# Performance work log

Measured on AMD Instinct MI355X. Metric: run time of the kernel, lower is better.

## Reference

```python
import jax, jax.numpy as jnp
import numpy as np

MARGIN = 0.35
SCALE = 64.0
EPS = 1e-8  # torch F.cosine_similarity norm clamp


def setup_inputs() -> dict:
    key = jax.random.key(0)
    k1, k2 = jax.random.split(key)
    N, D = 8192, 512
    embeddings = jax.random.normal(k1, (N, D), dtype=jnp.float32)
    labels = jax.random.randint(k2, (N,), 0, 128, dtype=jnp.int64)
    return {"embeddings": embeddings, "labels": labels}


def reference(embeddings, labels):
    # cosine similarity as Gram matrix of norm-clamped-normalized rows
    norms = jnp.maximum(jnp.linalg.norm(embeddings, axis=1, keepdims=True), EPS)
    e = embeddings / norms                      # [N, D]
    sim = jnp.einsum('id,jd->ij', e, e)         # [N, N]
    pos_mask = (labels[:, None] == labels[None, :]).astype(sim.dtype)
    # pos_sim - neg_sim = sim*mask - sim*(1-mask) = sim*(2*mask - 1)
    signed = sim * (2.0 * pos_mask - 1.0)
    loss = jnp.log1p(jnp.exp(-SCALE * (signed - MARGIN)))
    return jnp.mean(loss)
```

## Files before the change

### kernel.cpp

```cpp
#include <hip/hip_runtime.h>


typedef unsigned short u16;
typedef unsigned int u32;
typedef __attribute__((ext_vector_type(4))) float f32x4;
typedef __attribute__((ext_vector_type(8))) short bf16x8;
typedef __attribute__((ext_vector_type(8))) u16 u16x8;

#define AS1 __attribute__((address_space(1)))
#define AS3 __attribute__((address_space(3)))

__global__ __launch_bounds__(256) void norm_bf16_k(
    const float* __restrict__ emb, u16* __restrict__ e, int N, int D) {
  const int wid = threadIdx.x >> 6, lane = threadIdx.x & 63;
  const int row = blockIdx.x * 4 + wid;
  if (row >= N) return;
  const float* p = emb + (size_t)row * D + lane * 8;
  f32x4 a = *(const f32x4*)p;
  f32x4 b = *(const f32x4*)(p + 4);
  float ss = 0.f;
#pragma unroll
  for (int i = 0; i < 4; ++i) ss += a[i] * a[i] + b[i] * b[i];
#pragma unroll
  for (int o = 32; o >= 1; o >>= 1) ss += __shfl_xor(ss, o, 64);
  const float inv = 1.0f / fmaxf(sqrtf(ss), 1e-8f);
  u16x8 hv;
#pragma unroll
  for (int i = 0; i < 8; ++i) {
    float x = (i < 4 ? a[i] : b[i - 4]) * inv;
    u32 u = __float_as_uint(x);
    u += 0x7FFFu + ((u >> 16) & 1u);
    hv[i] = (u16)(u >> 16);
  }
  *(u16x8*)(e + (size_t)row * D + lane * 8) = hv;
}

__global__ __launch_bounds__(256, 4) void gram_loss_k(
    const u16* __restrict__ e, const int* __restrict__ labels,
    float* __restrict__ partials, int N, int D, int NT) {
  __shared__ __attribute__((aligned(16))) u16 sA[2][8 * 512];
  __shared__ __attribute__((aligned(16))) u16 sB[2][8 * 512];
  __shared__ float swred[4];

  const int tid = threadIdx.x, wid = tid >> 6, lane = tid & 63;

  int I = 0, rem = blockIdx.x, rl = NT;
  while (rem >= rl) { rem -= rl; ++I; --rl; }
  const int J = I + rem;
  const int i0 = I * 128, j0 = J * 128;

  const int rbase = (wid < 2) ? i0 : j0;
  const int fq0 = (wid & 1) * 4;
  u32 goff[4];
#pragma unroll
  for (int q = 0; q < 4; ++q)
    goff[q] = (u32)(rbase + (fq0 + q) * 16 + (lane & 15)) * (u32)D +
              ((lane >> 4) * 8);

  const f32x4 z = {0.f, 0.f, 0.f, 0.f};
  f32x4 acc[4][4];
#pragma unroll
  for (int m = 0; m < 4; ++m)
#pragma unroll
    for (int n = 0; n < 4; ++n) acc[m][n] = z;

  const int wr = wid >> 1, wc = wid & 1;

  auto stage = [&](int buf, int kk) {
    u16* dst = ((wid < 2) ? sA[buf] : sB[buf]) + fq0 * 512;
#pragma unroll
    for (int q = 0; q < 4; ++q)
      __builtin_amdgcn_global_load_lds((const AS1 void*)(e + goff[q] + kk),
                                       (AS3 void*)(dst + q * 512), 16, 0, 0);
  };
  auto compute = [&](int buf) {
    bf16x8 a[4], b[4];
#pragma unroll
    for (int m = 0; m < 4; ++m)
      a[m] = *(const bf16x8*)&sA[buf][(wr * 4 + m) * 512 + lane * 8];
#pragma unroll
    for (int n = 0; n < 4; ++n)
      b[n] = *(const bf16x8*)&sB[buf][(wc * 4 + n) * 512 + lane * 8];
#pragma unroll
    for (int m = 0; m < 4; ++m)
#pragma unroll
      for (int n = 0; n < 4; ++n)
        acc[m][n] =
            __builtin_amdgcn_mfma_f32_16x16x32_bf16(a[m], b[n], acc[m][n], 0, 0, 0);
  };

  stage(0, 0);
  __syncthreads();

#pragma unroll 2
  for (int t = 0; t < 15; ++t) {
    const int cur = t & 1;
    stage(cur ^ 1, (t + 1) * 32);
    compute(cur);
    __syncthreads();
  }
  compute(1);

  const float C0 = 64.0f * 0.35f;
  float lsum = 0.f;
  const int rb = i0 + wr * 64, cb = j0 + wc * 64;
#pragma unroll
  for (int m = 0; m < 4; ++m) {
    const int gi0 = rb + m * 16 + (lane >> 4) * 4;
#pragma unroll
    for (int n = 0; n < 4; ++n) {
      const int gj = cb + n * 16 + (lane & 15);
      const int lj = labels[gj];
#pragma unroll
      for (int r = 0; r < 4; ++r) {
        const int li = labels[gi0 + r];
        float s = acc[m][n][r];
        float sg = (li == lj) ? s : -s;
        float x = fmaf(-64.0f, sg, C0);
        float ax = fabsf(x);
        lsum += fmaxf(x, 0.f) + __logf(1.0f + __expf(-ax));
      }
    }
  }

#pragma unroll
  for (int o = 32; o >= 1; o >>= 1) lsum += __shfl_xor(lsum, o, 64);
  if (lane == 0) swred[wid] = lsum;
  __syncthreads();
  if (tid == 0) {
    float t = swred[0] + swred[1] + swred[2] + swred[3];
    partials[blockIdx.x] = (I == J) ? t : 2.0f * t;
  }
}

__global__ __launch_bounds__(256) void reduce_k(const float* __restrict__ partials,
                                                int n, float* __restrict__ out,
                                                double invNN) {
  double s = 0.0;
  for (int i = threadIdx.x; i < n; i += 256) s += (double)partials[i];
#pragma unroll
  for (int o = 32; o >= 1; o >>= 1) s += __shfl_xor(s, o, 64);
  __shared__ double sd[4];
  const int wid = threadIdx.x >> 6, lane = threadIdx.x & 63;
  if (lane == 0) sd[wid] = s;
  __syncthreads();
  if (threadIdx.x == 0) out[0] = (float)((sd[0] + sd[1] + sd[2] + sd[3]) * invNN);
}

extern "C" void kernel_launch(void* const* d_in, const int* in_sizes, int n_in,
                              void* d_out, int out_size, void* d_ws, size_t ws_size,
                              hipStream_t stream) {
  const float* emb = (const float*)d_in[0];
  const int* labels = (const int*)d_in[1];
  float* out = (float*)d_out;

  const int N = in_sizes[1];
  const int D = in_sizes[0] / N;
  const int NT = N / 128;
  const int nTiles = NT * (NT + 1) / 2;

  u16* e = (u16*)d_ws;
  float* partials = (float*)(e + (size_t)N * D);

  norm_bf16_k<<<N / 4, 256, 0, stream>>>(emb, e, N, D);
  gram_loss_k<<<nTiles, 256, 0, stream>>>(e, labels, partials, N, D, NT);
  reduce_k<<<1, 256, 0, stream>>>(partials, nTiles, out,
                                  1.0 / ((double)N * (double)N));
}
```

Measured before the change: 145.7 us.

## Triple-buffer K pipeline with vmcnt waits and XCD-aware tile remap

Replaces the double-buffered LDS loop with a three-stage ring that keeps up to two global-to-LDS loads in flight, using explicit s_waitcnt vmcnt counts and raw barriers instead of __syncthreads. It also remaps blockIdx so that round-robin dispatch across the eight XCDs gives each XCD a contiguous range of triangular tiles, improving L2 reuse of shared row panels. LDS use rises to 48KB per block and occupancy hint drops to 3 blocks per CU, trading occupancy for deeper prefetch.

Measured after the change: 143.4 us. Within noise of the previous version (-1.6%).

```diff
diff --git a/kernel.cpp b/kernel.cpp
--- a/kernel.cpp
+++ b/kernel.cpp
@@ -35,16 +35,20 @@
   *(u16x8*)(e + (size_t)row * D + lane * 8) = hv;
 }
 
-__global__ __launch_bounds__(256, 4) void gram_loss_k(
+__global__ __launch_bounds__(256, 3) void gram_loss_k(
     const u16* __restrict__ e, const int* __restrict__ labels,
-    float* __restrict__ partials, int N, int D, int NT) {
-  __shared__ __attribute__((aligned(16))) u16 sA[2][8 * 512];
-  __shared__ __attribute__((aligned(16))) u16 sB[2][8 * 512];
+    float* __restrict__ partials, int N, int D, int NT, int nwg) {
+  __shared__ __attribute__((aligned(16))) u16 sA[3][8 * 512];
+  __shared__ __attribute__((aligned(16))) u16 sB[3][8 * 512];
   __shared__ float swred[4];
 
   const int tid = threadIdx.x, wid = tid >> 6, lane = tid & 63;
 
-  int I = 0, rem = blockIdx.x, rl = NT;
+  const int q8 = nwg >> 3, r8 = nwg & 7;
+  const int x = blockIdx.x & 7, p = blockIdx.x >> 3;
+  const int bid = (x < r8 ? x * (q8 + 1) : r8 * (q8 + 1) + (x - r8) * q8) + p;
+
+  int I = 0, rem = bid, rl = NT;
   while (rem >= rl) { rem -= rl; ++I; --rl; }
   const int J = I + rem;
   const int i0 = I * 128, j0 = J * 128;
@@ -53,9 +57,9 @@
   const int fq0 = (wid & 1) * 4;
   u32 goff[4];
 #pragma unroll
-  for (int q = 0; q < 4; ++q)
-    goff[q] = (u32)(rbase + (fq0 + q) * 16 + (lane & 15)) * (u32)D +
-              ((lane >> 4) * 8);
+  for (int qq = 0; qq < 4; ++qq)
+    goff[qq] = (u32)(rbase + (fq0 + qq) * 16 + (lane & 15)) * (u32)D +
+               ((lane >> 4) * 8);
 
   const f32x4 z = {0.f, 0.f, 0.f, 0.f};
   f32x4 acc[4][4];
@@ -69,9 +73,9 @@
   auto stage = [&](int buf, int kk) {
     u16* dst = ((wid < 2) ? sA[buf] : sB[buf]) + fq0 * 512;
 #pragma unroll
-    for (int q = 0; q < 4; ++q)
-      __builtin_amdgcn_global_load_lds((const AS1 void*)(e + goff[q] + kk),
-                                       (AS3 void*)(dst + q * 512), 16, 0, 0);
+    for (int qq = 0; qq < 4; ++qq)
+      __builtin_amdgcn_global_load_lds((const AS1 void*)(e + goff[qq] + kk),
+                                       (AS3 void*)(dst + qq * 512), 16, 0, 0);
   };
   auto compute = [&](int buf) {
     bf16x8 a[4], b[4];
@@ -90,16 +94,22 @@
   };
 
   stage(0, 0);
-  __syncthreads();
+  stage(1, 32);
+  stage(2, 64);
 
-#pragma unroll 2
-  for (int t = 0; t < 15; ++t) {
-    const int cur = t & 1;
-    stage(cur ^ 1, (t + 1) * 32);
-    compute(cur);
-    __syncthreads();
-  }
-  compute(1);
+#define STEP(T, VM)                                          \
+  asm volatile("s_waitcnt vmcnt(" #VM ")" ::: "memory");     \
+  __builtin_amdgcn_s_barrier();                              \
+  asm volatile("" ::: "memory");                             \
+  compute((T) % 3);                                          \
+  __builtin_amdgcn_s_barrier();                              \
+  if ((T) + 3 < 16) stage((T) % 3, ((T) + 3) * 32);
+
+  STEP(0, 8)  STEP(1, 8)  STEP(2, 8)  STEP(3, 8)
+  STEP(4, 8)  STEP(5, 8)  STEP(6, 8)  STEP(7, 8)
+  STEP(8, 8)  STEP(9, 8)  STEP(10, 8) STEP(11, 8)
+  STEP(12, 8) STEP(13, 8) STEP(14, 4) STEP(15, 0)
+#undef STEP
 
   const float C0 = 64.0f * 0.35f;
   float lsum = 0.f;
@@ -116,9 +126,9 @@
         const int li = labels[gi0 + r];
         float s = acc[m][n][r];
         float sg = (li == lj) ? s : -s;
-        float x = fmaf(-64.0f, sg, C0);
-        float ax = fabsf(x);
-        lsum += fmaxf(x, 0.f) + __logf(1.0f + __expf(-ax));
+        float xv = fmaf(-64.0f, sg, C0);
+        float ax = fabsf(xv);
+        lsum += fmaxf(xv, 0.f) + __logf(1.0f + __expf(-ax));
       }
     }
   }
@@ -129,7 +139,7 @@
   __syncthreads();
   if (tid == 0) {
     float t = swred[0] + swred[1] + swred[2] + swred[3];
-    partials[blockIdx.x] = (I == J) ? t : 2.0f * t;
+    partials[bid] = (I == J) ? t : 2.0f * t;
   }
 }
 
@@ -163,7 +173,7 @@
   float* partials = (float*)(e + (size_t)N * D);
 
   norm_bf16_k<<<N / 4, 256, 0, stream>>>(emb, e, N, D);
-  gram_loss_k<<<nTiles, 256, 0, stream>>>(e, labels, partials, N, D, NT);
+  gram_loss_k<<<nTiles, 256, 0, stream>>>(e, labels, partials, N, D, NT, nTiles);
   reduce_k<<<1, 256, 0, stream>>>(partials, nTiles, out,
                                   1.0 / ((double)N * (double)N));
 }
```
